# Optimization experiments

Measured on AMD Instinct MI355X. Metric: run time of the kernel, lower is better.

The kernel has to match this reference:

```python
import jax, jax.numpy as jnp
import numpy as np

B, SV, SA, D, H, L, F = 1, 2048, 512, 1024, 16, 2, 4096
DH = D // H
S = SV + SA


def layer_norm(x):
    mu = jnp.mean(x, axis=-1, keepdims=True)
    var = jnp.var(x, axis=-1, keepdims=True)
    return (x - mu) * jax.lax.rsqrt(var + 1e-6)


def rms_norm(x, g):
    return x * jax.lax.rsqrt(jnp.mean(x * x, axis=-1, keepdims=True) + 1e-6) * g


def rope(x, theta):
    # x: [B,S,H*DH], theta: [S, DH//2] angles; complex-pair rotation as in rope_apply
    b, s, _ = x.shape
    x4 = x.reshape(b, s, H, DH)
    xe, xo = x4[..., 0::2], x4[..., 1::2]
    c = jnp.cos(theta)[None, :, None, :]
    sn = jnp.sin(theta)[None, :, None, :]
    re = xe * c - xo * sn
    im = xe * sn + xo * c
    return jnp.stack([re, im], axis=-1).reshape(b, s, H * DH)


def setup_inputs() -> dict:
    key = jax.random.key(0)
    ks = jax.random.split(key, 20)
    w = 0.02
    inp = {
        'video_tokens': jax.random.normal(ks[0], (B, SV, D), jnp.float32),
        'action_tokens': jax.random.normal(ks[1], (B, SA, D), jnp.float32),
        'video_freqs': jax.random.uniform(ks[2], (SV, DH // 2), jnp.float32) * 6.28,
        'action_freqs': jax.random.uniform(ks[3], (SA, DH // 2), jnp.float32) * 6.28,
        'video_t_mod': jax.random.normal(ks[4], (B, 6, D), jnp.float32),
        'action_t_mod': jax.random.normal(ks[5], (B, 6, D), jnp.float32),
        'Wq': jax.random.normal(ks[6], (2, L, D, D), jnp.float32) * w,
        'Wk': jax.random.normal(ks[7], (2, L, D, D), jnp.float32) * w,
        'Wv': jax.random.normal(ks[8], (2, L, D, D), jnp.float32) * w,
        'Wo': jax.random.normal(ks[9], (2, L, D, D), jnp.float32) * w,
        'bq': jnp.zeros((2, L, D), jnp.float32),
        'bk': jnp.zeros((2, L, D), jnp.float32),
        'bv': jnp.zeros((2, L, D), jnp.float32),
        'bo': jnp.zeros((2, L, D), jnp.float32),
        'gq': jnp.ones((2, L, D), jnp.float32),
        'gk': jnp.ones((2, L, D), jnp.float32),
        'mod': jax.random.normal(ks[10], (2, L, 6, D), jnp.float32) * 0.02,
        'W1': jax.random.normal(ks[11], (2, L, D, F), jnp.float32) * w,
        'b1': jnp.zeros((2, L, F), jnp.float32),
        'W2': jax.random.normal(ks[12], (2, L, F, D), jnp.float32) * w,
        'b2': jnp.zeros((2, L, D), jnp.float32),
    }
    # Mixed-modality ctx_mask: video bidirectional; action attends video + causal over action
    m = np.zeros((S, S), dtype=bool)
    m[:SV, :SV] = True
    m[SV:, :SV] = True
    m[SV:, SV:] = np.tril(np.ones((SA, SA), dtype=bool))
    inp['attention_mask'] = jnp.asarray(m)
    return inp


def _mot_forward(video_tokens, action_tokens, video_freqs, action_freqs,
                 video_t_mod, action_t_mod, Wq, Wk, Wv, Wo, bq, bk, bv, bo,
                 gq, gk, mod, W1, b1, W2, b2, attention_mask):
    xs = [video_tokens, action_tokens]
    thetas = [video_freqs, action_freqs]
    tmods = [video_t_mod, action_t_mod]
    scale = 1.0 / jnp.sqrt(jnp.asarray(DH, xs[0].dtype))
    for l in range(L):
        qs, kss, vs, posts = [], [], [], []
        for e in range(2):
            m6 = mod[e, l][None] + tmods[e]  # [B,6,D]
            sh_msa, sc_msa, g_msa, sh_mlp, sc_mlp, g_mlp = (
                m6[:, i:i + 1, :] for i in range(6))
            a = layer_norm(xs[e]) * (1.0 + sc_msa) + sh_msa
            q = rope(rms_norm(a @ Wq[e, l] + bq[e, l], gq[e, l]), thetas[e])
            k = rope(rms_norm(a @ Wk[e, l] + bk[e, l], gk[e, l]), thetas[e])
            v = a @ Wv[e, l] + bv[e, l]
            qs.append(q); kss.append(k); vs.append(v)
            posts.append((g_msa, sh_mlp, sc_mlp, g_mlp))
        qc = jnp.concatenate(qs, axis=1).reshape(B, S, H, DH)
        kc = jnp.concatenate(kss, axis=1).reshape(B, S, H, DH)
        vc = jnp.concatenate(vs, axis=1).reshape(B, S, H, DH)
        scores = jnp.einsum('bqhd,bkhd->bhqk', qc, kc) * scale
        scores = jnp.where(attention_mask[None, None], scores, -1e9)
        p = jax.nn.softmax(scores, axis=-1)
        o = jnp.einsum('bhqk,bkhd->bqhd', p, vc).reshape(B, S, H * DH)
        outs = [o[:, :SV], o[:, SV:]]
        for e in range(2):
            g_msa, sh_mlp, sc_mlp, g_mlp = posts[e]
            x = xs[e] + g_msa * (outs[e] @ Wo[e, l] + bo[e, l])
            mi = layer_norm(x) * (1.0 + sc_mlp) + sh_mlp
            h = jax.nn.gelu(mi @ W1[e, l] + b1[e, l], approximate=True) @ W2[e, l] + b2[e, l]
            xs[e] = x + g_mlp * h
    return jnp.concatenate(xs, axis=1)  # [B, SV+SA, D]


def reference(video_tokens, action_tokens, video_freqs, action_freqs,
              video_t_mod, action_t_mod, Wq, Wk, Wv, Wo, bq, bk, bv, bo,
              gq, gk, mod, W1, b1, W2, b2, attention_mask):
    return _mot_forward(video_tokens, action_tokens, video_freqs, action_freqs,
                        video_t_mod, action_t_mod, Wq, Wk, Wv, Wo, bq, bk, bv, bo,
                        gq, gk, mod, W1, b1, W2, b2, attention_mask)
```

## Files before the change

kernel.cpp:

```cpp
#include <hip/hip_runtime.h>
#include <hip/hip_bf16.h>

#define BF16 __hip_bfloat16
typedef short bf16x8 __attribute__((ext_vector_type(8)));
typedef float f32x4  __attribute__((ext_vector_type(4)));
typedef unsigned int u32;

#define MFMA16(a, b, c) __builtin_amdgcn_mfma_f32_16x16x32_bf16(a, b, c, 0, 0, 0)


__device__ __forceinline__ void async16(const void* g, void* l) {
  __builtin_amdgcn_global_load_lds(
      (const __attribute__((address_space(1))) u32*)g,
      (__attribute__((address_space(3))) u32*)l, 16, 0, 0);
}

__device__ __forceinline__ u32 pkbf(float a, float b) {
  union { BF16 h; unsigned short s; } ua, ub;
  ua.h = __float2bfloat16(a); ub.h = __float2bfloat16(b);
  return (u32)ua.s | ((u32)ub.s << 16);
}

__global__ __launch_bounds__(256) void wtrans(const float* __restrict__ W,
                                              BF16* __restrict__ WT, int K, int N,
                                              size_t outZ) {
  __shared__ float t[32][33];
  const float* Wm = W + (size_t)K * N * blockIdx.z;
  BF16* Tm = WT + outZ * blockIdx.z;
  int n0 = blockIdx.x * 32, k0 = blockIdx.y * 32;
  int tx = threadIdx.x & 31, ty = threadIdx.x >> 5;
#pragma unroll
  for (int i = 0; i < 4; i++)
    t[ty + 8 * i][tx] = Wm[(size_t)(k0 + ty + 8 * i) * N + n0 + tx];
  __syncthreads();
#pragma unroll
  for (int i = 0; i < 4; i++)
    Tm[(size_t)(n0 + ty + 8 * i) * K + k0 + tx] = __float2bfloat16(t[tx][ty + 8 * i]);
}

__global__ __launch_bounds__(256) void packb(const float* __restrict__ bq,
                                             const float* __restrict__ bk,
                                             const float* __restrict__ bv,
                                             float* __restrict__ bqkv) {
  int i = blockIdx.x * 256 + threadIdx.x;
  int s = i / 3072, c = i - s * 3072;
  float v = (c < 1024) ? bq[s * 1024 + c]
          : (c < 2048) ? bk[s * 1024 + c - 1024]
                       : bv[s * 1024 + c - 2048];
  bqkv[i] = v;
}

__global__ __launch_bounds__(256) void ln_mod(const float* __restrict__ x,
                                              BF16* __restrict__ out,
                                              const float* __restrict__ mod,
                                              const float* __restrict__ tmv,
                                              const float* __restrict__ tma,
                                              int l, int ish, int isc) {
  int r = blockIdx.x;
  int e = (r >= 2048) ? 1 : 0;
  const float* tm = e ? tma : tmv;
  const float* mo = mod + (size_t)((e * 2 + l) * 6) * 1024;
  float4 v = ((const float4*)(x + (size_t)r * 1024))[threadIdx.x];
  float s = v.x + v.y + v.z + v.w;
  float s2 = v.x * v.x + v.y * v.y + v.z * v.z + v.w * v.w;
#pragma unroll
  for (int off = 32; off >= 1; off >>= 1) {
    s += __shfl_down(s, off);
    s2 += __shfl_down(s2, off);
  }
  __shared__ float red[8];
  int lane = threadIdx.x & 63, w = threadIdx.x >> 6;
  if (lane == 0) { red[w] = s; red[4 + w] = s2; }
  __syncthreads();
  s = red[0] + red[1] + red[2] + red[3];
  s2 = red[4] + red[5] + red[6] + red[7];
  float mu = s * (1.f / 1024.f);
  float var = s2 * (1.f / 1024.f) - mu * mu;
  float inv = rsqrtf(var + 1e-6f);
  int c = threadIdx.x * 4;
  BF16* o = out + (size_t)r * 1024 + c;
  float xv[4] = {v.x, v.y, v.z, v.w};
#pragma unroll
  for (int k = 0; k < 4; k++) {
    float sc = mo[isc * 1024 + c + k] + tm[isc * 1024 + c + k];
    float sh = mo[ish * 1024 + c + k] + tm[ish * 1024 + c + k];
    o[k] = __float2bfloat16((xv[k] - mu) * inv * (1.f + sc) + sh);
  }
}

__global__ __launch_bounds__(256) void qk_post(const float* __restrict__ qkv,
                                               const float* __restrict__ gq,
                                               const float* __restrict__ gk,
                                               BF16* __restrict__ Qb, BF16* __restrict__ Kb,
                                               const float* __restrict__ vfreq,
                                               const float* __restrict__ afreq, int l) {
  int r = blockIdx.x;
  int which = blockIdx.y;
  const float* src = qkv + (size_t)r * 3072 + which * 1024;
  int e = (r >= 2048) ? 1 : 0;
  const float* g = (which ? gk : gq) + (size_t)(e * 2 + l) * 1024;
  BF16* dst = which ? Kb : Qb;
  const float* fr = e ? (afreq + (size_t)(r - 2048) * 32) : (vfreq + (size_t)r * 32);
  float4 v = ((const float4*)src)[threadIdx.x];
  float s2 = v.x * v.x + v.y * v.y + v.z * v.z + v.w * v.w;
#pragma unroll
  for (int off = 32; off >= 1; off >>= 1) s2 += __shfl_down(s2, off);
  __shared__ float red[4];
  int lane = threadIdx.x & 63, w = threadIdx.x >> 6;
  if (lane == 0) red[w] = s2;
  __syncthreads();
  s2 = red[0] + red[1] + red[2] + red[3];
  float inv = rsqrtf(s2 * (1.f / 1024.f) + 1e-6f);
  if (which == 0) inv *= 0.125f * 1.44269504f;
  int c = threadIdx.x * 4;
  float xe0 = v.x * inv * g[c], xo0 = v.y * inv * g[c + 1];
  float xe1 = v.z * inv * g[c + 2], xo1 = v.w * inv * g[c + 3];
  int p0 = (c & 63) >> 1;
  float c0, s0, c1, s1;
  __sincosf(fr[p0], &s0, &c0);
  __sincosf(fr[p0 + 1], &s1, &c1);
  int h = c >> 6;
  size_t o = ((size_t)h * 2560 + r) * 64 + (c & 63);
  dst[o + 0] = __float2bfloat16(xe0 * c0 - xo0 * s0);
  dst[o + 1] = __float2bfloat16(xe0 * s0 + xo0 * c0);
  dst[o + 2] = __float2bfloat16(xe1 * c1 - xo1 * s1);
  dst[o + 3] = __float2bfloat16(xe1 * s1 + xo1 * c1);
}

__global__ __launch_bounds__(256) void vpost(const float* __restrict__ qkv,
                                             BF16* __restrict__ VT) {
  __shared__ float t[32][33];
  int r0 = blockIdx.x * 32, c0 = blockIdx.y * 32;
  int tx = threadIdx.x & 31, ty = threadIdx.x >> 5;
#pragma unroll
  for (int i = 0; i < 4; i++)
    t[ty + 8 * i][tx] = qkv[(size_t)(r0 + ty + 8 * i) * 3072 + 2048 + c0 + tx];
  __syncthreads();
#pragma unroll
  for (int i = 0; i < 4; i++)
    VT[(size_t)(c0 + ty + 8 * i) * 2560 + r0 + tx] = __float2bfloat16(t[tx][ty + 8 * i]);
}

template <int EPI, int KS>
__global__ __launch_bounds__(256) void gemm2(const BF16* __restrict__ A,
                                             const BF16* __restrict__ Bw, size_t Bestride,
                                             const float* __restrict__ bias, int biasE,
                                             void* __restrict__ out, float* __restrict__ part,
                                             int N, int K) {
  __shared__ BF16 As[128 * 64];
  __shared__ BF16 Bs[128 * 64];
  int flat = blockIdx.x + blockIdx.y * gridDim.x;
  int xcd = flat & 7, slot = flat >> 3;
  int bx = slot % gridDim.x;
  int by = (slot / gridDim.x) * 8 + xcd;
  int m0 = bx * 128, n0 = by * 128;
  int e = (m0 >= 2048);
  const BF16* Ab = A + (size_t)m0 * K;
  const BF16* Bb = Bw + (e ? Bestride : 0) + (size_t)n0 * K;
  int kz0 = blockIdx.z * (K / KS), kz1 = kz0 + K / KS;
  int tid = threadIdx.x, lane = tid & 63, w = tid >> 6;
  int wr = w & 1, wc = w >> 1;
  int m15 = lane & 15, q4 = lane >> 4;
  int L[4], rS[4], cS[4];
#pragma unroll
  for (int i = 0; i < 4; i++) {
    L[i] = w * 256 + i * 64 + lane;
    rS[i] = L[i] >> 3;
    cS[i] = (L[i] & 7) ^ (rS[i] & 7);
  }
  f32x4 acc[4][4] = {};
  for (int k0 = kz0; k0 < kz1; k0 += 64) {
    __syncthreads();
#pragma unroll
    for (int i = 0; i < 4; i++) {
      async16(Ab + (size_t)rS[i] * K + k0 + cS[i] * 8, &As[L[i] * 8]);
      async16(Bb + (size_t)rS[i] * K + k0 + cS[i] * 8, &Bs[L[i] * 8]);
    }
    __syncthreads();
#pragma unroll
    for (int kk = 0; kk < 2; kk++) {
      int pos = ((kk * 4 + q4) ^ (m15 & 7)) * 8;
      bf16x8 af[4], bv[4];
#pragma unroll
      for (int i = 0; i < 4; i++) af[i] = *(const bf16x8*)&As[(wr * 64 + i * 16 + m15) * 64 + pos];
#pragma unroll
      for (int j = 0; j < 4; j++) bv[j] = *(const bf16x8*)&Bs[(wc * 64 + j * 16 + m15) * 64 + pos];
#pragma unroll
      for (int i = 0; i < 4; i++)
#pragma unroll
        for (int j = 0; j < 4; j++)
          acc[i][j] = MFMA16(af[i], bv[j], acc[i][j]);
    }
  }
#pragma unroll
  for (int i = 0; i < 4; i++) {
    int row = m0 + wr * 64 + 16 * i + q4 * 4;
#pragma unroll
    for (int j = 0; j < 4; j++) {
      int col = n0 + wc * 64 + 16 * j + m15;
      float b = (EPI == 3) ? 0.f : bias[e * biasE + col];
#pragma unroll
      for (int rg = 0; rg < 4; rg++) {
        float v = acc[i][j][rg] + b;
        size_t idx = (size_t)(row + rg) * N + col;
        if (EPI == 0) {
          ((float*)out)[idx] = v;
        } else if (EPI == 1) {
          float u = 0.7978845608f * (v + 0.044715f * v * v * v);
          ((BF16*)out)[idx] = __float2bfloat16(0.5f * v * (1.f + tanhf(u)));
        } else {
          part[(size_t)blockIdx.z * 2560 * N + idx] = v;
        }
      }
    }
  }
}

template <int KS>
__global__ __launch_bounds__(256) void combine(const float* __restrict__ part,
                                               const float* __restrict__ biasL,
                                               const float* __restrict__ modp, int gi, int l,
                                               const float* __restrict__ tmv,
                                               const float* __restrict__ tma,
                                               const float* __restrict__ xin,
                                               float* __restrict__ xout) {
  int r = blockIdx.x, e = (r >= 2048) ? 1 : 0;
  int c = threadIdx.x * 4;
  float4 s = {0.f, 0.f, 0.f, 0.f};
#pragma unroll
  for (int z = 0; z < KS; z++) {
    float4 p = *(const float4*)&part[((size_t)z * 2560 + r) * 1024 + c];
    s.x += p.x; s.y += p.y; s.z += p.z; s.w += p.w;
  }
  float4 b = *(const float4*)&biasL[e * 2048 + c];
  const float* tm = e ? tma : tmv;
  float4 gm = *(const float4*)&modp[(size_t)((e * 2 + l) * 6 + gi) * 1024 + c];
  float4 gt = *(const float4*)&tm[gi * 1024 + c];
  float4 xi = *(const float4*)&xin[(size_t)r * 1024 + c];
  float4 o;
  o.x = xi.x + (gm.x + gt.x) * (s.x + b.x);
  o.y = xi.y + (gm.y + gt.y) * (s.y + b.y);
  o.z = xi.z + (gm.z + gt.z) * (s.z + b.z);
  o.w = xi.w + (gm.w + gt.w) * (s.w + b.w);
  *(float4*)&xout[(size_t)r * 1024 + c] = o;
}

__global__ __launch_bounds__(256) void flash3(const BF16* __restrict__ Qb,
                                              const BF16* __restrict__ Kb,
                                              const BF16* __restrict__ VT,
                                              BF16* __restrict__ O) {
  const int S = 2560;
  __shared__ BF16 Ks[2][64 * 64];
  __shared__ BF16 Vs[2][64 * 64];
  __shared__ BF16 Ps[4][16 * 72];
  int tid = threadIdx.x, lane = tid & 63, w = tid >> 6;
  int h = blockIdx.y, q0 = blockIdx.x * 64;
  int m15 = lane & 15, q4 = lane >> 4;
  int actq = (q0 >= 2048);
  int nt = actq ? ((q0 >> 6) + 1) : 32;
  const BF16* qrow = Qb + ((size_t)h * S + q0 + w * 16 + m15) * 64;
  bf16x8 qf0 = *(const bf16x8*)(qrow + q4 * 8);
  bf16x8 qf1 = *(const bf16x8*)(qrow + 32 + q4 * 8);
  const BF16* kbase = Kb + (size_t)h * S * 64;
  const BF16* vbase = VT + (size_t)h * 64 * S;
  int L0 = w * 128 + lane, L1 = L0 + 64;
  int r0 = L0 >> 3, c0 = (L0 & 7) ^ (r0 & 7);
  int r1 = L1 >> 3, c1 = (L1 & 7) ^ (r1 & 7);
  async16(kbase + (size_t)r0 * 64 + c0 * 8, &Ks[0][L0 * 8]);
  async16(kbase + (size_t)r1 * 64 + c1 * 8, &Ks[0][L1 * 8]);
  async16(vbase + (size_t)r0 * S + c0 * 8, &Vs[0][L0 * 8]);
  async16(vbase + (size_t)r1 * S + c1 * 8, &Vs[0][L1 * 8]);
  f32x4 oa[4] = {};
  float m_i = -1e30f, l_i = 0.f;
  int colq = q0 + w * 16 + m15;
  BF16* Pw = &Ps[w][0];
  int x0 = (q4 ^ (m15 & 7)) * 8, x1 = ((4 + q4) ^ (m15 & 7)) * 8;
  __syncthreads();
  for (int t = 0; t < nt; t++) {
    int cur = t & 1;
    if (t + 1 < nt) {
      int nb = cur ^ 1;
      const BF16* kg = kbase + (size_t)(t + 1) * 64 * 64;
      const BF16* vg = vbase + (size_t)(t + 1) * 64;
      async16(kg + (size_t)r0 * 64 + c0 * 8, &Ks[nb][L0 * 8]);
      async16(kg + (size_t)r1 * 64 + c1 * 8, &Ks[nb][L1 * 8]);
      async16(vg + (size_t)r0 * S + c0 * 8, &Vs[nb][L0 * 8]);
      async16(vg + (size_t)r1 * S + c1 * 8, &Vs[nb][L1 * 8]);
    }
    f32x4 st[4];
#pragma unroll
    for (int jt = 0; jt < 4; jt++) {
      int row = (jt * 16 + m15) * 64;
      bf16x8 kf0 = *(const bf16x8*)&Ks[cur][row + x0];
      bf16x8 kf1 = *(const bf16x8*)&Ks[cur][row + x1];
      f32x4 z = {};
      z = MFMA16(kf0, qf0, z);
      st[jt] = MFMA16(kf1, qf1, z);
    }
    float mx = -1e30f;
    if (actq && t == nt - 1) {
#pragma unroll
      for (int jt = 0; jt < 4; jt++)
#pragma unroll
        for (int rg = 0; rg < 4; rg++) {
          int rowkv = t * 64 + jt * 16 + q4 * 4 + rg;
          if (rowkv > colq) st[jt][rg] = -1e30f;
          mx = fmaxf(mx, st[jt][rg]);
        }
    } else {
#pragma unroll
      for (int jt = 0; jt < 4; jt++)
        mx = fmaxf(fmaxf(fmaxf(mx, st[jt][0]), fmaxf(st[jt][1], st[jt][2])), st[jt][3]);
    }
    mx = fmaxf(mx, __shfl_xor(mx, 16));
    mx = fmaxf(mx, __shfl_xor(mx, 32));
    float mn = fmaxf(m_i, mx);
    float al = exp2f(m_i - mn);
    m_i = mn;
    float rs = 0.f;
#pragma unroll
    for (int jt = 0; jt < 4; jt++) {
      float p0 = exp2f(st[jt][0] - mn), p1 = exp2f(st[jt][1] - mn);
      float p2 = exp2f(st[jt][2] - mn), p3 = exp2f(st[jt][3] - mn);
      rs += (p0 + p1) + (p2 + p3);
      uint2 pr = {pkbf(p0, p1), pkbf(p2, p3)};
      *(uint2*)&Pw[m15 * 72 + jt * 16 + q4 * 4] = pr;
    }
    rs += __shfl_xor(rs, 16);
    rs += __shfl_xor(rs, 32);
    l_i = l_i * al + rs;
    float alr[4];
#pragma unroll
    for (int rg = 0; rg < 4; rg++) alr[rg] = __shfl(al, q4 * 4 + rg);
#pragma unroll
    for (int dt = 0; dt < 4; dt++)
#pragma unroll
      for (int rg = 0; rg < 4; rg++) oa[dt][rg] *= alr[rg];
    bf16x8 pf0 = *(const bf16x8*)&Pw[m15 * 72 + q4 * 8];
    bf16x8 pf1 = *(const bf16x8*)&Pw[m15 * 72 + 32 + q4 * 8];
#pragma unroll
    for (int dt = 0; dt < 4; dt++) {
      int vr = (dt * 16 + m15) * 64;
      bf16x8 vf0 = *(const bf16x8*)&Vs[cur][vr + x0];
      bf16x8 vf1 = *(const bf16x8*)&Vs[cur][vr + x1];
      oa[dt] = MFMA16(pf0, vf0, oa[dt]);
      oa[dt] = MFMA16(pf1, vf1, oa[dt]);
    }
    __syncthreads();
  }
  float rl = 1.f / l_i;
  float rlr[4];
#pragma unroll
  for (int rg = 0; rg < 4; rg++) rlr[rg] = __shfl(rl, q4 * 4 + rg);
#pragma unroll
  for (int dt = 0; dt < 4; dt++)
#pragma unroll
    for (int rg = 0; rg < 4; rg++) {
      int row = q0 + w * 16 + q4 * 4 + rg;
      int col = h * 64 + dt * 16 + m15;
      O[(size_t)row * 1024 + col] = __float2bfloat16(oa[dt][rg] * rlr[rg]);
    }
}

extern "C" void kernel_launch(void* const* d_in, const int* in_sizes, int n_in,
                              void* d_out, int out_size, void* d_ws, size_t ws_size,
                              hipStream_t stream) {
  (void)in_sizes; (void)n_in; (void)out_size; (void)ws_size;
  const float* vid  = (const float*)d_in[0];
  const float* act  = (const float*)d_in[1];
  const float* vfr  = (const float*)d_in[2];
  const float* afr  = (const float*)d_in[3];
  const float* tmv  = (const float*)d_in[4];
  const float* tma  = (const float*)d_in[5];
  const float* Wq   = (const float*)d_in[6];
  const float* Wk   = (const float*)d_in[7];
  const float* Wv   = (const float*)d_in[8];
  const float* Wo   = (const float*)d_in[9];
  const float* bq   = (const float*)d_in[10];
  const float* bk   = (const float*)d_in[11];
  const float* bv   = (const float*)d_in[12];
  const float* bo   = (const float*)d_in[13];
  const float* gq   = (const float*)d_in[14];
  const float* gk   = (const float*)d_in[15];
  const float* modp = (const float*)d_in[16];
  const float* W1   = (const float*)d_in[17];
  const float* b1   = (const float*)d_in[18];
  const float* W2   = (const float*)d_in[19];
  const float* b2   = (const float*)d_in[20];

  char* p = (char*)d_ws;
  auto carve = [&](size_t bytes) {
    char* r = p;
    p += (bytes + 255) & ~(size_t)255;
    return r;
  };
  BF16* WqkvT = (BF16*)carve(4ull * 3072 * 1024 * 2);
  BF16* WoT   = (BF16*)carve(4ull * 1024 * 1024 * 2);
  BF16* W1T   = (BF16*)carve(4ull * 4096 * 1024 * 2);
  BF16* W2T   = (BF16*)carve(4ull * 1024 * 4096 * 2);
  float* bqkv = (float*)carve(4ull * 3072 * 4);
  float* x    = (float*)carve(2560ull * 1024 * 4);
  BF16* abf   = (BF16*)carve(2560ull * 1024 * 2);
  float* qkv  = (float*)carve(2560ull * 3072 * 4);
  BF16* Qb    = (BF16*)carve(2560ull * 1024 * 2);
  BF16* Kb    = (BF16*)carve(2560ull * 1024 * 2);
  float* part = qkv;
  BF16* VTb   = (BF16*)carve(2560ull * 1024 * 2);
  BF16* Obf   = (BF16*)carve(2560ull * 1024 * 2);
  BF16* mibf  = (BF16*)carve(2560ull * 1024 * 2);
  BF16* hbf   = (BF16*)carve(2560ull * 4096 * 2);

  hipMemcpyAsync(x, vid, 2048ull * 1024 * 4, hipMemcpyDeviceToDevice, stream);
  hipMemcpyAsync(x + 2048ull * 1024, act, 512ull * 1024 * 4, hipMemcpyDeviceToDevice, stream);

  const size_t S3 = 3072ull * 1024;
  wtrans<<<dim3(32, 32, 4), 256, 0, stream>>>(Wq, WqkvT, 1024, 1024, S3);
  wtrans<<<dim3(32, 32, 4), 256, 0, stream>>>(Wk, WqkvT + 1024ull * 1024, 1024, 1024, S3);
  wtrans<<<dim3(32, 32, 4), 256, 0, stream>>>(Wv, WqkvT + 2048ull * 1024, 1024, 1024, S3);
  wtrans<<<dim3(32, 32, 4), 256, 0, stream>>>(Wo, WoT, 1024, 1024, 1024ull * 1024);
  wtrans<<<dim3(128, 32, 4), 256, 0, stream>>>(W1, W1T, 1024, 4096, 4096ull * 1024);
  wtrans<<<dim3(32, 128, 4), 256, 0, stream>>>(W2, W2T, 4096, 1024, 1024ull * 4096);
  packb<<<48, 256, 0, stream>>>(bq, bk, bv, bqkv);

  for (int l = 0; l < 2; l++) {
    ln_mod<<<2560, 256, 0, stream>>>(x, abf, modp, tmv, tma, l, 0, 1);
    gemm2<0, 1><<<dim3(20, 24, 1), 256, 0, stream>>>(
        abf, WqkvT + (size_t)l * S3, 2 * S3, bqkv + l * 3072, 6144, qkv, nullptr, 3072, 1024);
    qk_post<<<dim3(2560, 2), 256, 0, stream>>>(qkv, gq, gk, Qb, Kb, vfr, afr, l);
    vpost<<<dim3(80, 32), 256, 0, stream>>>(qkv, VTb);
    flash3<<<dim3(40, 16), 256, 0, stream>>>(Qb, Kb, VTb, Obf);
    gemm2<3, 2><<<dim3(20, 8, 2), 256, 0, stream>>>(
        Obf, WoT + (size_t)l * 1024 * 1024, 2ull * 1024 * 1024, nullptr, 0, nullptr, part,
        1024, 1024);
    combine<2><<<2560, 256, 0, stream>>>(part, bo + l * 1024, modp, 2, l, tmv, tma, x, x);
    ln_mod<<<2560, 256, 0, stream>>>(x, mibf, modp, tmv, tma, l, 3, 4);
    gemm2<1, 1><<<dim3(20, 32, 1), 256, 0, stream>>>(
        mibf, W1T + (size_t)l * 4096 * 1024, 2ull * 4096 * 1024, b1 + l * 4096, 8192, hbf,
        nullptr, 4096, 1024);
    gemm2<3, 4><<<dim3(20, 8, 4), 256, 0, stream>>>(
        hbf, W2T + (size_t)l * 4096 * 1024, 2ull * 4096 * 1024, nullptr, 0, nullptr, part,
        1024, 4096);
    combine<4><<<2560, 256, 0, stream>>>(part, b2 + l * 1024, modp, 5, l, tmv, tma, x,
                                         (l == 1) ? (float*)d_out : x);
  }
}
```

Measured before the change: 783.9 us.

## Split attention KV range across two blocks and merge partials in combine kernel

Flash attention now splits each query tile's key/value range in half across a new grid z dimension, writing unnormalized fp32 partial outputs plus per-row max and sum, and a new combine kernel merges them into bf16 output. This doubles the block count from 640 to 1280 to fill more compute units, at the cost of extra global traffic and an extra launch. It also adds lazy rescaling that skips the output rescale when the running max grows by at most 8, and swaps the padded P buffer for an XOR-swizzled layout in shared memory.

Result: faster. 757.7 us (-3.3%).

```diff
diff --git a/kernel.cpp b/kernel.cpp
--- a/kernel.cpp
+++ b/kernel.cpp
@@ -245,19 +245,22 @@
   *(float4*)&xout[(size_t)r * 1024 + c] = o;
 }
 
-__global__ __launch_bounds__(256) void flash3(const BF16* __restrict__ Qb,
+__global__ __launch_bounds__(256) void flash4(const BF16* __restrict__ Qb,
                                               const BF16* __restrict__ Kb,
                                               const BF16* __restrict__ VT,
-                                              BF16* __restrict__ O) {
+                                              float* __restrict__ Op,
+                                              float* __restrict__ ml) {
   const int S = 2560;
   __shared__ BF16 Ks[2][64 * 64];
   __shared__ BF16 Vs[2][64 * 64];
-  __shared__ BF16 Ps[4][16 * 72];
+  __shared__ BF16 Ps[4][16 * 64];
   int tid = threadIdx.x, lane = tid & 63, w = tid >> 6;
-  int h = blockIdx.y, q0 = blockIdx.x * 64;
+  int h = blockIdx.y, q0 = blockIdx.x * 64, kz = blockIdx.z;
   int m15 = lane & 15, q4 = lane >> 4;
   int actq = (q0 >= 2048);
   int nt = actq ? ((q0 >> 6) + 1) : 32;
+  int tb = kz ? (nt >> 1) : 0;
+  int te = kz ? nt : (nt >> 1);
   const BF16* qrow = Qb + ((size_t)h * S + q0 + w * 16 + m15) * 64;
   bf16x8 qf0 = *(const bf16x8*)(qrow + q4 * 8);
   bf16x8 qf1 = *(const bf16x8*)(qrow + 32 + q4 * 8);
@@ -266,19 +269,25 @@
   int L0 = w * 128 + lane, L1 = L0 + 64;
   int r0 = L0 >> 3, c0 = (L0 & 7) ^ (r0 & 7);
   int r1 = L1 >> 3, c1 = (L1 & 7) ^ (r1 & 7);
-  async16(kbase + (size_t)r0 * 64 + c0 * 8, &Ks[0][L0 * 8]);
-  async16(kbase + (size_t)r1 * 64 + c1 * 8, &Ks[0][L1 * 8]);
-  async16(vbase + (size_t)r0 * S + c0 * 8, &Vs[0][L0 * 8]);
-  async16(vbase + (size_t)r1 * S + c1 * 8, &Vs[0][L1 * 8]);
+  {
+    const BF16* kg = kbase + (size_t)tb * 64 * 64;
+    const BF16* vg = vbase + (size_t)tb * 64;
+    async16(kg + (size_t)r0 * 64 + c0 * 8, &Ks[0][L0 * 8]);
+    async16(kg + (size_t)r1 * 64 + c1 * 8, &Ks[0][L1 * 8]);
+    async16(vg + (size_t)r0 * S + c0 * 8, &Vs[0][L0 * 8]);
+    async16(vg + (size_t)r1 * S + c1 * 8, &Vs[0][L1 * 8]);
+  }
   f32x4 oa[4] = {};
   float m_i = -1e30f, l_i = 0.f;
   int colq = q0 + w * 16 + m15;
-  BF16* Pw = &Ps[w][0];
+  char* Pw = (char*)&Ps[w][0];
+  int prow = m15 * 128;
+  int pswz = (m15 & 7) << 4;
   int x0 = (q4 ^ (m15 & 7)) * 8, x1 = ((4 + q4) ^ (m15 & 7)) * 8;
   __syncthreads();
-  for (int t = 0; t < nt; t++) {
-    int cur = t & 1;
-    if (t + 1 < nt) {
+  for (int t = tb; t < te; t++) {
+    int cur = (t - tb) & 1;
+    if (t + 1 < te) {
       int nb = cur ^ 1;
       const BF16* kg = kbase + (size_t)(t + 1) * 64 * 64;
       const BF16* vg = vbase + (size_t)(t + 1) * 64;
@@ -293,9 +302,9 @@
       int row = (jt * 16 + m15) * 64;
       bf16x8 kf0 = *(const bf16x8*)&Ks[cur][row + x0];
       bf16x8 kf1 = *(const bf16x8*)&Ks[cur][row + x1];
-      f32x4 z = {};
-      z = MFMA16(kf0, qf0, z);
-      st[jt] = MFMA16(kf1, qf1, z);
+      f32x4 zz = {};
+      zz = MFMA16(kf0, qf0, zz);
+      st[jt] = MFMA16(kf1, qf1, zz);
     }
     float mx = -1e30f;
     if (actq && t == nt - 1) {
@@ -309,35 +318,40 @@
         }
     } else {
 #pragma unroll
-      for (int jt = 0; jt < 4; jt++)
-        mx = fmaxf(fmaxf(fmaxf(mx, st[jt][0]), fmaxf(st[jt][1], st[jt][2])), st[jt][3]);
+      for (int jt = 0; jt < 4; jt++) {
+        mx = fmaxf(fmaxf(mx, st[jt][0]), st[jt][1]);
+        mx = fmaxf(fmaxf(mx, st[jt][2]), st[jt][3]);
+      }
     }
     mx = fmaxf(mx, __shfl_xor(mx, 16));
     mx = fmaxf(mx, __shfl_xor(mx, 32));
-    float mn = fmaxf(m_i, mx);
-    float al = exp2f(m_i - mn);
-    m_i = mn;
+    if (!__all(mx <= m_i + 8.f)) {
+      float mn = fmaxf(m_i, mx);
+      float al = exp2f(m_i - mn);
+      m_i = mn;
+      l_i *= al;
+      float alr[4];
+#pragma unroll
+      for (int rg = 0; rg < 4; rg++) alr[rg] = __shfl(al, q4 * 4 + rg);
+#pragma unroll
+      for (int dt = 0; dt < 4; dt++)
+#pragma unroll
+        for (int rg = 0; rg < 4; rg++) oa[dt][rg] *= alr[rg];
+    }
     float rs = 0.f;
 #pragma unroll
     for (int jt = 0; jt < 4; jt++) {
-      float p0 = exp2f(st[jt][0] - mn), p1 = exp2f(st[jt][1] - mn);
-      float p2 = exp2f(st[jt][2] - mn), p3 = exp2f(st[jt][3] - mn);
+      float p0 = exp2f(st[jt][0] - m_i), p1 = exp2f(st[jt][1] - m_i);
+      float p2 = exp2f(st[jt][2] - m_i), p3 = exp2f(st[jt][3] - m_i);
       rs += (p0 + p1) + (p2 + p3);
       uint2 pr = {pkbf(p0, p1), pkbf(p2, p3)};
-      *(uint2*)&Pw[m15 * 72 + jt * 16 + q4 * 4] = pr;
+      *(uint2*)(Pw + prow + ((jt * 32 + q4 * 8) ^ pswz)) = pr;
     }
     rs += __shfl_xor(rs, 16);
     rs += __shfl_xor(rs, 32);
-    l_i = l_i * al + rs;
-    float alr[4];
-#pragma unroll
-    for (int rg = 0; rg < 4; rg++) alr[rg] = __shfl(al, q4 * 4 + rg);
-#pragma unroll
-    for (int dt = 0; dt < 4; dt++)
-#pragma unroll
-      for (int rg = 0; rg < 4; rg++) oa[dt][rg] *= alr[rg];
-    bf16x8 pf0 = *(const bf16x8*)&Pw[m15 * 72 + q4 * 8];
-    bf16x8 pf1 = *(const bf16x8*)&Pw[m15 * 72 + 32 + q4 * 8];
+    l_i += rs;
+    bf16x8 pf0 = *(const bf16x8*)(Pw + prow + ((q4 * 16) ^ pswz));
+    bf16x8 pf1 = *(const bf16x8*)(Pw + prow + ((64 + q4 * 16) ^ pswz));
 #pragma unroll
     for (int dt = 0; dt < 4; dt++) {
       int vr = (dt * 16 + m15) * 64;
@@ -348,18 +362,45 @@
     }
     __syncthreads();
   }
-  float rl = 1.f / l_i;
-  float rlr[4];
-#pragma unroll
-  for (int rg = 0; rg < 4; rg++) rlr[rg] = __shfl(rl, q4 * 4 + rg);
+  size_t ob = (((size_t)kz * 16 + h) * 40 + blockIdx.x) * 4096;
 #pragma unroll
   for (int dt = 0; dt < 4; dt++)
 #pragma unroll
-    for (int rg = 0; rg < 4; rg++) {
-      int row = q0 + w * 16 + q4 * 4 + rg;
-      int col = h * 64 + dt * 16 + m15;
-      O[(size_t)row * 1024 + col] = __float2bfloat16(oa[dt][rg] * rlr[rg]);
-    }
+    for (int rg = 0; rg < 4; rg++)
+      Op[ob + (size_t)(w * 16 + q4 * 4 + rg) * 64 + dt * 16 + m15] = oa[dt][rg];
+  if (q4 == 0) {
+    float* mp = ml + (((size_t)kz * 16 + h) * 40 + blockIdx.x) * 128;
+    mp[w * 16 + m15] = m_i;
+    mp[64 + w * 16 + m15] = l_i;
+  }
+}
+
+__global__ __launch_bounds__(256) void fcomb(const float* __restrict__ Op,
+                                             const float* __restrict__ ml,
+                                             BF16* __restrict__ O) {
+  int qt = blockIdx.x, h = blockIdx.y;
+  int q = threadIdx.x >> 2;
+  int d0 = (threadIdx.x & 3) * 16;
+  size_t tile = (size_t)h * 40 + qt;
+  const size_t zO = (size_t)16 * 40 * 4096;
+  const size_t zm = (size_t)16 * 40 * 128;
+  size_t base = tile * 4096 + (size_t)q * 64 + d0;
+  size_t mb = tile * 128 + q;
+  float m0 = ml[mb], l0 = ml[mb + 64];
+  float m1 = ml[zm + mb], l1 = ml[zm + mb + 64];
+  float M = fmaxf(m0, m1);
+  float a = exp2f(m0 - M), b = exp2f(m1 - M);
+  float r = 1.f / (a * l0 + b * l1);
+  a *= r; b *= r;
+  BF16* orow = O + (size_t)(qt * 64 + q) * 1024 + h * 64 + d0;
+#pragma unroll
+  for (int i = 0; i < 4; i++) {
+    float4 x0 = *(const float4*)&Op[base + i * 4];
+    float4 x1 = *(const float4*)&Op[zO + base + i * 4];
+    uint2 pr = {pkbf(a * x0.x + b * x1.x, a * x0.y + b * x1.y),
+                pkbf(a * x0.z + b * x1.z, a * x0.w + b * x1.w)};
+    *(uint2*)(orow + i * 4) = pr;
+  }
 }
 
 extern "C" void kernel_launch(void* const* d_in, const int* in_sizes, int n_in,
@@ -405,6 +446,8 @@
   BF16* Qb    = (BF16*)carve(2560ull * 1024 * 2);
   BF16* Kb    = (BF16*)carve(2560ull * 1024 * 2);
   float* part = qkv;
+  float* Opar = qkv;
+  float* mlb  = qkv + 2ull * 16 * 40 * 4096;
   BF16* VTb   = (BF16*)carve(2560ull * 1024 * 2);
   BF16* Obf   = (BF16*)carve(2560ull * 1024 * 2);
   BF16* mibf  = (BF16*)carve(2560ull * 1024 * 2);
@@ -428,7 +471,8 @@
         abf, WqkvT + (size_t)l * S3, 2 * S3, bqkv + l * 3072, 6144, qkv, nullptr, 3072, 1024);
     qk_post<<<dim3(2560, 2), 256, 0, stream>>>(qkv, gq, gk, Qb, Kb, vfr, afr, l);
     vpost<<<dim3(80, 32), 256, 0, stream>>>(qkv, VTb);
-    flash3<<<dim3(40, 16), 256, 0, stream>>>(Qb, Kb, VTb, Obf);
+    flash4<<<dim3(40, 16, 2), 256, 0, stream>>>(Qb, Kb, VTb, Opar, mlb);
+    fcomb<<<dim3(40, 16), 256, 0, stream>>>(Opar, mlb, Obf);
     gemm2<3, 2><<<dim3(20, 8, 2), 256, 0, stream>>>(
         Obf, WoT + (size_t)l * 1024 * 1024, 2ull * 1024 * 1024, nullptr, 0, nullptr, part,
         1024, 1024);
```
